# Optimization experiments

Measured on AMD Instinct MI355X. Metric: run time of the kernel, lower is better.

The kernel has to match this reference:

```python
import jax, jax.numpy as jnp
import numpy as np

N = 1024
OBS_RADIUS = 0.5


def setup_inputs() -> dict:
    key = jax.random.key(0)
    ks = jax.random.split(key, 16)
    def w(k, shape, fan_in):
        return jax.random.normal(k, shape, dtype=jnp.float32) / np.sqrt(fan_in).astype(np.float32)
    return {
        "s": jax.random.normal(ks[0], (N, 4), dtype=jnp.float32),
        "g": jax.random.normal(ks[1], (N, 2), dtype=jnp.float32),
        "conv1_w": w(ks[2], (64, 5), 5),   "conv1_b": jnp.zeros((64,), jnp.float32),
        "conv2_w": w(ks[3], (128, 64), 64), "conv2_b": jnp.zeros((128,), jnp.float32),
        "fc1_w": w(ks[4], (64, 132), 132), "fc1_b": jnp.zeros((64,), jnp.float32),
        "fc2_w": w(ks[5], (128, 64), 64),  "fc2_b": jnp.zeros((128,), jnp.float32),
        "fc3_w": w(ks[6], (64, 128), 128), "fc3_b": jnp.zeros((64,), jnp.float32),
        "fc4_w": w(ks[7], (4, 64), 64),    "fc4_b": jnp.zeros((4,), jnp.float32),
    }


def reference(s, g, conv1_w, conv1_b, conv2_w, conv2_b,
              fc1_w, fc1_b, fc2_w, fc2_b, fc3_w, fc3_b, fc4_w, fc4_b):
    n = s.shape[0]
    # pairwise agent diff + identity channel: [n, n, 5]
    pd = s[:, None, :] - s[None, :, :]
    x = jnp.concatenate([pd, jnp.eye(n, dtype=s.dtype)[:, :, None]], axis=2)
    # neighbor mask from positional distance: [n, n, 1]
    dist = jnp.linalg.norm(x[:, :, :2], axis=2, keepdims=True)
    mask = (dist < OBS_RADIUS).astype(s.dtype)
    # 1x1-conv edge MLPs (pointwise over the j dim): [n, n, 64] -> [n, n, 128]
    h = jax.nn.relu(jnp.einsum('ijc,oc->ijo', x, conv1_w) + conv1_b)
    h = jax.nn.relu(jnp.einsum('ijc,oc->ijo', h, conv2_w) + conv2_b)
    # masked max-pool over neighbors j: [n, 128]
    pooled = jnp.max(h * mask, axis=1)
    sg = s[:, :2] - g
    feat = jnp.concatenate([pooled, sg, s[:, 2:]], axis=1)  # [n, 132]
    z = jax.nn.relu(feat @ fc1_w.T + fc1_b)
    z = jax.nn.relu(z @ fc2_w.T + fc2_b)
    z = jax.nn.relu(z @ fc3_w.T + fc3_b)
    k = 2.0 * jax.nn.sigmoid(z @ fc4_w.T + fc4_b) - 1.0  # [n, 4]
    k1, k2, k3, k4 = k[:, 0:1], k[:, 1:2], k[:, 2:3], k[:, 3:4]
    zr = jnp.zeros_like(k1)
    gain_x = -jnp.concatenate([k1, zr, k2, zr], axis=1)
    gain_y = -jnp.concatenate([zr, k3, zr, k4], axis=1)
    state = jnp.concatenate([sg, s[:, 2:]], axis=1)  # [n, 4]
    a_x = jnp.sum(state * gain_x, axis=1, keepdims=True)
    a_y = jnp.sum(state * gain_y, axis=1, keepdims=True)
    return jnp.concatenate([a_x, a_y], axis=1)  # [n, 2]
```

## Files before the change

### kernel.cpp

```cpp
#include <hip/hip_runtime.h>

typedef unsigned int u32;
typedef unsigned short u16;
typedef _Float16 f16;
typedef f16 f16x8 __attribute__((ext_vector_type(8)));
typedef float f32x4 __attribute__((ext_vector_type(4)));

#define SH1 72

__global__ __launch_bounds__(64) void NetworkAction_86131274154571_kernel(
    const float* __restrict__ s,    const float* __restrict__ g,
    const float* __restrict__ w1g,  const float* __restrict__ b1g,
    const float* __restrict__ w2g,  const float* __restrict__ b2g,
    const float* __restrict__ fc1w, const float* __restrict__ fc1b,
    const float* __restrict__ fc2w, const float* __restrict__ fc2b,
    const float* __restrict__ fc3w, const float* __restrict__ fc3b,
    const float* __restrict__ fc4w, const float* __restrict__ fc4b,
    float2* __restrict__ out)
{
    __shared__ float4 actx[1024];
    __shared__ float  actf[1024];
    __shared__ f16    h1buf[16][SH1];
    __shared__ float  feat[132];
    __shared__ float  z1[64];
    __shared__ float  z2[128];
    __shared__ float  z3[64];
    __shared__ float  kk[4];

    const int lane = threadIdx.x;
    const int i    = blockIdx.x;
    const int ncol = lane & 15;
    const int kq   = lane >> 4;

    const float4 si = ((const float4*)s)[i];

    const float* wp1 = w1g + lane * 5;
    const float w10 = wp1[0], w11 = wp1[1], w12 = wp1[2], w13 = wp1[3], w14 = wp1[4];
    const float b1r = b1g[lane];

    f16x8 bfrag[8][2];
    float b2r[8];
    #pragma unroll
    for (int tile = 0; tile < 8; ++tile) {
        const int n = tile * 16 + ncol;
        b2r[tile] = b2g[n];
        #pragma unroll
        for (int t = 0; t < 2; ++t) {
            const float* wp = w2g + n * 64 + t * 32 + kq * 8;
            float4 lo = ((const float4*)wp)[0];
            float4 hi = ((const float4*)wp)[1];
            f16x8 b;
            b[0] = (f16)lo.x; b[1] = (f16)lo.y; b[2] = (f16)lo.z; b[3] = (f16)lo.w;
            b[4] = (f16)hi.x; b[5] = (f16)hi.y; b[6] = (f16)hi.z; b[7] = (f16)hi.w;
            bfrag[tile][t] = b;
        }
    }

    int cnt = 0;
    #pragma unroll
    for (int it = 0; it < 16; ++it) {
        const int j = it * 64 + lane;
        float4 sj = ((const float4*)s)[j];
        float dx = si.x - sj.x, dy = si.y - sj.y;
        bool act = (dx * dx + dy * dy) < 0.25f;
        unsigned long long m = __ballot(act);
        if (act) {
            int pos = cnt + (int)__popcll(m & ((1ull << lane) - 1ull));
            actx[pos] = make_float4(dx, dy, si.z - sj.z, si.w - sj.w);
            actf[pos] = (j == i) ? 1.0f : 0.0f;
        }
        cnt += (int)__popcll(m);
    }
    const int n_act = cnt;
    __syncthreads();

    float mt[8];
    #pragma unroll
    for (int t = 0; t < 8; ++t) mt[t] = 0.0f;

    for (int gbase = 0; gbase < n_act; gbase += 16) {
        #pragma unroll
        for (int p = 0; p < 16; ++p) {
            if (gbase + p < n_act) {
                const float4 x  = actx[gbase + p];
                const float  x4 = actf[gbase + p];
                float h = b1r;
                h = fmaf(w10, x.x, h); h = fmaf(w11, x.y, h);
                h = fmaf(w12, x.z, h); h = fmaf(w13, x.w, h);
                h = fmaf(w14, x4,  h);
                h1buf[p][lane] = (f16)fmaxf(h, 0.0f);
            }
        }
        __syncthreads();

        f16x8 afr[2];
        #pragma unroll
        for (int t = 0; t < 2; ++t)
            afr[t] = *(const f16x8*)&h1buf[ncol][t * 32 + kq * 8];

        #pragma unroll
        for (int tile = 0; tile < 8; ++tile) {
            f32x4 acc = {0.0f, 0.0f, 0.0f, 0.0f};
            acc = __builtin_amdgcn_mfma_f32_16x16x32_f16(afr[0], bfrag[tile][0], acc, 0, 0, 0);
            acc = __builtin_amdgcn_mfma_f32_16x16x32_f16(afr[1], bfrag[tile][1], acc, 0, 0, 0);
            #pragma unroll
            for (int r = 0; r < 4; ++r) {
                const bool valid = (gbase + kq * 4 + r) < n_act;
                const float v = acc[r] + b2r[tile];
                mt[tile] = valid ? fmaxf(mt[tile], v) : mt[tile];
            }
        }
        __syncthreads();
    }

    #pragma unroll
    for (int tile = 0; tile < 8; ++tile) {
        float m = mt[tile];
        m = fmaxf(m, __shfl_xor(m, 16));
        m = fmaxf(m, __shfl_xor(m, 32));
        if (lane < 16) feat[tile * 16 + lane] = m;
    }
    if (lane == 0) {
        float2 gi = ((const float2*)g)[i];
        feat[128] = si.x - gi.x;
        feat[129] = si.y - gi.y;
        feat[130] = si.z;
        feat[131] = si.w;
    }
    __syncthreads();

    {
        float a0 = fc1b[lane], a1 = 0.f, a2 = 0.f, a3 = 0.f;
        const float4* wv = (const float4*)(fc1w + lane * 132);
        #pragma unroll
        for (int q = 0; q < 33; ++q) {
            float4 u = wv[q];
            const int k = q * 4;
            float* a = (q & 3) == 0 ? &a0 : (q & 3) == 1 ? &a1 : (q & 3) == 2 ? &a2 : &a3;
            *a = fmaf(u.x, feat[k + 0], *a);
            *a = fmaf(u.y, feat[k + 1], *a);
            *a = fmaf(u.z, feat[k + 2], *a);
            *a = fmaf(u.w, feat[k + 3], *a);
        }
        z1[lane] = fmaxf((a0 + a1) + (a2 + a3), 0.0f);
    }
    __syncthreads();

    {
        float aA0 = fc2b[lane],      aA1 = 0.f;
        float aB0 = fc2b[lane + 64], aB1 = 0.f;
        const float4* wvA = (const float4*)(fc2w + lane * 64);
        const float4* wvB = (const float4*)(fc2w + (lane + 64) * 64);
        #pragma unroll
        for (int q = 0; q < 16; ++q) {
            float4 uA = wvA[q];
            float4 uB = wvB[q];
            const int k = q * 4;
            const float f0 = z1[k + 0], f1 = z1[k + 1], f2 = z1[k + 2], f3 = z1[k + 3];
            if (q & 1) {
                aA1 = fmaf(uA.x, f0, aA1); aA1 = fmaf(uA.y, f1, aA1);
                aA1 = fmaf(uA.z, f2, aA1); aA1 = fmaf(uA.w, f3, aA1);
                aB1 = fmaf(uB.x, f0, aB1); aB1 = fmaf(uB.y, f1, aB1);
                aB1 = fmaf(uB.z, f2, aB1); aB1 = fmaf(uB.w, f3, aB1);
            } else {
                aA0 = fmaf(uA.x, f0, aA0); aA0 = fmaf(uA.y, f1, aA0);
                aA0 = fmaf(uA.z, f2, aA0); aA0 = fmaf(uA.w, f3, aA0);
                aB0 = fmaf(uB.x, f0, aB0); aB0 = fmaf(uB.y, f1, aB0);
                aB0 = fmaf(uB.z, f2, aB0); aB0 = fmaf(uB.w, f3, aB0);
            }
        }
        z2[lane]      = fmaxf(aA0 + aA1, 0.0f);
        z2[lane + 64] = fmaxf(aB0 + aB1, 0.0f);
    }
    __syncthreads();

    {
        float a0 = fc3b[lane], a1 = 0.f, a2 = 0.f, a3 = 0.f;
        const float4* wv = (const float4*)(fc3w + lane * 128);
        #pragma unroll
        for (int q = 0; q < 32; ++q) {
            float4 u = wv[q];
            const int k = q * 4;
            float* a = (q & 3) == 0 ? &a0 : (q & 3) == 1 ? &a1 : (q & 3) == 2 ? &a2 : &a3;
            *a = fmaf(u.x, z2[k + 0], *a);
            *a = fmaf(u.y, z2[k + 1], *a);
            *a = fmaf(u.z, z2[k + 2], *a);
            *a = fmaf(u.w, z2[k + 3], *a);
        }
        z3[lane] = fmaxf((a0 + a1) + (a2 + a3), 0.0f);
    }
    __syncthreads();

    {
        const int q  = lane >> 4;
        const int ks = lane & 15;
        float4 u = ((const float4*)(fc4w + q * 64))[ks];
        float part = u.x * z3[ks * 4 + 0] + u.y * z3[ks * 4 + 1]
                   + u.z * z3[ks * 4 + 2] + u.w * z3[ks * 4 + 3];
        part += __shfl_xor(part, 1);
        part += __shfl_xor(part, 2);
        part += __shfl_xor(part, 4);
        part += __shfl_xor(part, 8);
        if (ks == 0)
            kk[q] = 2.0f / (1.0f + expf(-(part + fc4b[q]))) - 1.0f;
    }
    __syncthreads();

    if (lane == 0) {
        float ax = -(kk[0] * feat[128] + kk[1] * feat[130]);
        float ay = -(kk[2] * feat[129] + kk[3] * feat[131]);
        out[i] = make_float2(ax, ay);
    }
}

extern "C" void kernel_launch(void* const* d_in, const int* in_sizes, int n_in,
                              void* d_out, int out_size, void* d_ws, size_t ws_size,
                              hipStream_t stream) {
    const float* s    = (const float*)d_in[0];
    const float* g    = (const float*)d_in[1];
    const float* c1w  = (const float*)d_in[2];
    const float* c1b  = (const float*)d_in[3];
    const float* c2w  = (const float*)d_in[4];
    const float* c2b  = (const float*)d_in[5];
    const float* fc1w = (const float*)d_in[6];
    const float* fc1b = (const float*)d_in[7];
    const float* fc2w = (const float*)d_in[8];
    const float* fc2b = (const float*)d_in[9];
    const float* fc3w = (const float*)d_in[10];
    const float* fc3b = (const float*)d_in[11];
    const float* fc4w = (const float*)d_in[12];
    const float* fc4b = (const float*)d_in[13];

    float2* out = (float2*)d_out;

    NetworkAction_86131274154571_kernel<<<1024, 64, 0, stream>>>(
        s, g, c1w, c1b, c2w, c2b, fc1w, fc1b, fc2w, fc2b,
        fc3w, fc3b, fc4w, fc4b, out);
}
```

Before: 105.6 us.

## Split neighbor scan across four waves with shared fp16 conv2 weights

Each block now launches four waves. Each wave scans a quarter of the candidate neighbors, compacts them into its own slice, and runs its own MFMA edge-MLP loop. Conv2 weights are converted to fp16 once into shared memory and read from there instead of being held as per-lane register fragments. Partial max-pools are combined through shared memory, after which wave 0 alone runs the FC head, using lgkmcnt waits and shuffles in place of block barriers. Work per row is spread over more waves, at the cost of extra LDS traffic for the B fragments and an idle three waves during the FC tail.

New measurement: 104.4 us. Within noise of the previous version (-1.2%).

```diff
diff --git a/kernel.cpp b/kernel.cpp
--- a/kernel.cpp
+++ b/kernel.cpp
@@ -6,9 +6,11 @@
 typedef f16 f16x8 __attribute__((ext_vector_type(8)));
 typedef float f32x4 __attribute__((ext_vector_type(4)));
 
+#define NTH 256
 #define SH1 72
-
-__global__ __launch_bounds__(64) void NetworkAction_86131274154571_kernel(
+#define SW2 72
+
+__global__ __launch_bounds__(NTH) void NetworkAction_86131274154571_kernel(
     const float* __restrict__ s,    const float* __restrict__ g,
     const float* __restrict__ w1g,  const float* __restrict__ b1g,
     const float* __restrict__ w2g,  const float* __restrict__ b2g,
@@ -19,71 +21,78 @@
     float2* __restrict__ out)
 {
     __shared__ float4 actx[1024];
-    __shared__ float  actf[1024];
-    __shared__ f16    h1buf[16][SH1];
+    __shared__ f16    w2s[128][SW2];
+    __shared__ f16    h1all[4][16][SH1];
+    __shared__ float  pmax[4][128];
+    __shared__ int    diagslot[4];
     __shared__ float  feat[132];
     __shared__ float  z1[64];
     __shared__ float  z2[128];
     __shared__ float  z3[64];
-    __shared__ float  kk[4];
-
-    const int lane = threadIdx.x;
+
+    const int tid  = threadIdx.x;
+    const int lane = tid & 63;
+    const int wave = tid >> 6;
     const int i    = blockIdx.x;
     const int ncol = lane & 15;
     const int kq   = lane >> 4;
 
     const float4 si = ((const float4*)s)[i];
 
+    if (lane == 0) diagslot[wave] = -1;
+
+    {
+        const int n = tid >> 1, h = tid & 1;
+        const float4* wp = (const float4*)(w2g + n * 64 + h * 32);
+        #pragma unroll
+        for (int q = 0; q < 8; q += 2) {
+            float4 u0 = wp[q], u1 = wp[q + 1];
+            f16x8 b;
+            b[0] = (f16)u0.x; b[1] = (f16)u0.y; b[2] = (f16)u0.z; b[3] = (f16)u0.w;
+            b[4] = (f16)u1.x; b[5] = (f16)u1.y; b[6] = (f16)u1.z; b[7] = (f16)u1.w;
+            *(f16x8*)&w2s[n][h * 32 + q * 4] = b;
+        }
+    }
+
     const float* wp1 = w1g + lane * 5;
     const float w10 = wp1[0], w11 = wp1[1], w12 = wp1[2], w13 = wp1[3], w14 = wp1[4];
     const float b1r = b1g[lane];
-
-    f16x8 bfrag[8][2];
     float b2r[8];
     #pragma unroll
-    for (int tile = 0; tile < 8; ++tile) {
-        const int n = tile * 16 + ncol;
-        b2r[tile] = b2g[n];
-        #pragma unroll
-        for (int t = 0; t < 2; ++t) {
-            const float* wp = w2g + n * 64 + t * 32 + kq * 8;
-            float4 lo = ((const float4*)wp)[0];
-            float4 hi = ((const float4*)wp)[1];
-            f16x8 b;
-            b[0] = (f16)lo.x; b[1] = (f16)lo.y; b[2] = (f16)lo.z; b[3] = (f16)lo.w;
-            b[4] = (f16)hi.x; b[5] = (f16)hi.y; b[6] = (f16)hi.z; b[7] = (f16)hi.w;
-            bfrag[tile][t] = b;
-        }
-    }
+    for (int t = 0; t < 8; ++t) b2r[t] = b2g[t * 16 + ncol];
 
     int cnt = 0;
-    #pragma unroll
-    for (int it = 0; it < 16; ++it) {
-        const int j = it * 64 + lane;
+    const int jbase = wave * 256;
+    #pragma unroll
+    for (int it = 0; it < 4; ++it) {
+        const int j = jbase + it * 64 + lane;
         float4 sj = ((const float4*)s)[j];
         float dx = si.x - sj.x, dy = si.y - sj.y;
         bool act = (dx * dx + dy * dy) < 0.25f;
         unsigned long long m = __ballot(act);
         if (act) {
             int pos = cnt + (int)__popcll(m & ((1ull << lane) - 1ull));
-            actx[pos] = make_float4(dx, dy, si.z - sj.z, si.w - sj.w);
-            actf[pos] = (j == i) ? 1.0f : 0.0f;
+            actx[jbase + pos] = make_float4(dx, dy, si.z - sj.z, si.w - sj.w);
+            if (j == i) diagslot[wave] = pos;
         }
         cnt += (int)__popcll(m);
     }
-    const int n_act = cnt;
     __syncthreads();
 
+    const int dslot = diagslot[wave];
+    const float4* actw = &actx[jbase];
+    f16 (*h1buf)[SH1] = h1all[wave];
+
     float mt[8];
     #pragma unroll
     for (int t = 0; t < 8; ++t) mt[t] = 0.0f;
 
-    for (int gbase = 0; gbase < n_act; gbase += 16) {
+    for (int gbase = 0; gbase < cnt; gbase += 16) {
         #pragma unroll
         for (int p = 0; p < 16; ++p) {
-            if (gbase + p < n_act) {
-                const float4 x  = actx[gbase + p];
-                const float  x4 = actf[gbase + p];
+            if (gbase + p < cnt) {
+                const float4 x  = actw[gbase + p];
+                const float  x4 = (gbase + p == dslot) ? 1.0f : 0.0f;
                 float h = b1r;
                 h = fmaf(w10, x.x, h); h = fmaf(w11, x.y, h);
                 h = fmaf(w12, x.z, h); h = fmaf(w13, x.w, h);
@@ -91,26 +100,26 @@
                 h1buf[p][lane] = (f16)fmaxf(h, 0.0f);
             }
         }
-        __syncthreads();
-
-        f16x8 afr[2];
-        #pragma unroll
-        for (int t = 0; t < 2; ++t)
-            afr[t] = *(const f16x8*)&h1buf[ncol][t * 32 + kq * 8];
+        asm volatile("s_waitcnt lgkmcnt(0)" ::: "memory");
+
+        f16x8 afr0 = *(const f16x8*)&h1buf[ncol][kq * 8];
+        f16x8 afr1 = *(const f16x8*)&h1buf[ncol][32 + kq * 8];
 
         #pragma unroll
         for (int tile = 0; tile < 8; ++tile) {
+            const int n = tile * 16 + ncol;
+            f16x8 b0 = *(const f16x8*)&w2s[n][kq * 8];
+            f16x8 b1 = *(const f16x8*)&w2s[n][32 + kq * 8];
             f32x4 acc = {0.0f, 0.0f, 0.0f, 0.0f};
-            acc = __builtin_amdgcn_mfma_f32_16x16x32_f16(afr[0], bfrag[tile][0], acc, 0, 0, 0);
-            acc = __builtin_amdgcn_mfma_f32_16x16x32_f16(afr[1], bfrag[tile][1], acc, 0, 0, 0);
+            acc = __builtin_amdgcn_mfma_f32_16x16x32_f16(afr0, b0, acc, 0, 0, 0);
+            acc = __builtin_amdgcn_mfma_f32_16x16x32_f16(afr1, b1, acc, 0, 0, 0);
             #pragma unroll
             for (int r = 0; r < 4; ++r) {
-                const bool valid = (gbase + kq * 4 + r) < n_act;
+                const bool valid = (gbase + kq * 4 + r) < cnt;
                 const float v = acc[r] + b2r[tile];
                 mt[tile] = valid ? fmaxf(mt[tile], v) : mt[tile];
             }
         }
-        __syncthreads();
     }
 
     #pragma unroll
@@ -118,16 +127,25 @@
         float m = mt[tile];
         m = fmaxf(m, __shfl_xor(m, 16));
         m = fmaxf(m, __shfl_xor(m, 32));
-        if (lane < 16) feat[tile * 16 + lane] = m;
-    }
+        if (lane < 16) pmax[wave][tile * 16 + lane] = m;
+    }
+    __syncthreads();
+    if (wave != 0) return;
+
+    {
+        float m0 = fmaxf(fmaxf(pmax[0][lane],      pmax[1][lane]),
+                         fmaxf(pmax[2][lane],      pmax[3][lane]));
+        float m1 = fmaxf(fmaxf(pmax[0][lane + 64], pmax[1][lane + 64]),
+                         fmaxf(pmax[2][lane + 64], pmax[3][lane + 64]));
+        feat[lane]      = m0;
+        feat[lane + 64] = m1;
+    }
+    const float2 gi = ((const float2*)g)[i];
+    const float sgx = si.x - gi.x, sgy = si.y - gi.y;
     if (lane == 0) {
-        float2 gi = ((const float2*)g)[i];
-        feat[128] = si.x - gi.x;
-        feat[129] = si.y - gi.y;
-        feat[130] = si.z;
-        feat[131] = si.w;
-    }
-    __syncthreads();
+        feat[128] = sgx; feat[129] = sgy; feat[130] = si.z; feat[131] = si.w;
+    }
+    asm volatile("s_waitcnt lgkmcnt(0)" ::: "memory");
 
     {
         float a0 = fc1b[lane], a1 = 0.f, a2 = 0.f, a3 = 0.f;
@@ -144,7 +162,7 @@
         }
         z1[lane] = fmaxf((a0 + a1) + (a2 + a3), 0.0f);
     }
-    __syncthreads();
+    asm volatile("s_waitcnt lgkmcnt(0)" ::: "memory");
 
     {
         float aA0 = fc2b[lane],      aA1 = 0.f;
@@ -172,7 +190,7 @@
         z2[lane]      = fmaxf(aA0 + aA1, 0.0f);
         z2[lane + 64] = fmaxf(aB0 + aB1, 0.0f);
     }
-    __syncthreads();
+    asm volatile("s_waitcnt lgkmcnt(0)" ::: "memory");
 
     {
         float a0 = fc3b[lane], a1 = 0.f, a2 = 0.f, a3 = 0.f;
@@ -189,7 +207,7 @@
         }
         z3[lane] = fmaxf((a0 + a1) + (a2 + a3), 0.0f);
     }
-    __syncthreads();
+    asm volatile("s_waitcnt lgkmcnt(0)" ::: "memory");
 
     {
         const int q  = lane >> 4;
@@ -201,15 +219,16 @@
         part += __shfl_xor(part, 2);
         part += __shfl_xor(part, 4);
         part += __shfl_xor(part, 8);
-        if (ks == 0)
-            kk[q] = 2.0f / (1.0f + expf(-(part + fc4b[q]))) - 1.0f;
-    }
-    __syncthreads();
-
-    if (lane == 0) {
-        float ax = -(kk[0] * feat[128] + kk[1] * feat[130]);
-        float ay = -(kk[2] * feat[129] + kk[3] * feat[131]);
-        out[i] = make_float2(ax, ay);
+        const float kv = 2.0f / (1.0f + expf(-(part + fc4b[q]))) - 1.0f;
+        const float k0 = __shfl(kv, 0);
+        const float k1 = __shfl(kv, 16);
+        const float k2 = __shfl(kv, 32);
+        const float k3 = __shfl(kv, 48);
+        if (lane == 0) {
+            float ax = -(k0 * sgx + k1 * si.z);
+            float ay = -(k2 * sgy + k3 * si.w);
+            out[i] = make_float2(ax, ay);
+        }
     }
 }
 
@@ -233,7 +252,7 @@
 
     float2* out = (float2*)d_out;
 
-    NetworkAction_86131274154571_kernel<<<1024, 64, 0, stream>>>(
+    NetworkAction_86131274154571_kernel<<<1024, NTH, 0, stream>>>(
         s, g, c1w, c1b, c2w, c2b, fc1w, fc1b, fc2w, fc2b,
         fc3w, fc3b, fc4w, fc4b, out);
 }
```

## Split edge MLP across four waves per block with double-buffered h1 staging

Applied to the files above, without the earlier changes.

Raises the block from one wave to four, so each wave owns 32 of the 128 conv2 output channels. The layer-1 computation for each group of 16 neighbors is spread over all 256 threads, each computing two channels from shared-memory weights. The h1 buffer is double-buffered so one barrier per group can be dropped. Neighbor compaction now uses a shared atomic counter instead of a wave ballot, and the diagonal slot is tracked rather than stored per entry. After pooling, the tail MLP runs on wave 0 only, using s_waitcnt instead of barriers and shuffles for the final gains. Per-block work is cut and occupancy raised, at the cost of more block-wide syncs and atomic contention.

After: 99.86 us. -5.5%, faster.

```diff
diff --git a/kernel.cpp b/kernel.cpp
--- a/kernel.cpp
+++ b/kernel.cpp
@@ -6,9 +6,10 @@
 typedef f16 f16x8 __attribute__((ext_vector_type(8)));
 typedef float f32x4 __attribute__((ext_vector_type(4)));
 
+#define NTH 256
 #define SH1 72
 
-__global__ __launch_bounds__(64) void NetworkAction_86131274154571_kernel(
+__global__ __launch_bounds__(NTH) void NetworkAction_86131274154571_kernel(
     const float* __restrict__ s,    const float* __restrict__ g,
     const float* __restrict__ w1g,  const float* __restrict__ b1g,
     const float* __restrict__ w2g,  const float* __restrict__ b2g,
@@ -19,30 +20,35 @@
     float2* __restrict__ out)
 {
     __shared__ float4 actx[1024];
-    __shared__ float  actf[1024];
-    __shared__ f16    h1buf[16][SH1];
+    __shared__ f16    h1buf[2][16][SH1];
+    __shared__ float  w1s[320];
+    __shared__ float  b1s[64];
     __shared__ float  feat[132];
     __shared__ float  z1[64];
     __shared__ float  z2[128];
     __shared__ float  z3[64];
-    __shared__ float  kk[4];
-
-    const int lane = threadIdx.x;
+    __shared__ int    cnt;
+    __shared__ int    diagslot;
+
+    const int tid  = threadIdx.x;
+    const int lane = tid & 63;
+    const int wave = tid >> 6;
     const int i    = blockIdx.x;
     const int ncol = lane & 15;
     const int kq   = lane >> 4;
 
+    if (tid == 0) cnt = 0;
+    for (int q = tid; q < 320; q += NTH) w1s[q] = w1g[q];
+    if (tid < 64) b1s[tid] = b1g[tid];
+
     const float4 si = ((const float4*)s)[i];
 
-    const float* wp1 = w1g + lane * 5;
-    const float w10 = wp1[0], w11 = wp1[1], w12 = wp1[2], w13 = wp1[3], w14 = wp1[4];
-    const float b1r = b1g[lane];
-
-    f16x8 bfrag[8][2];
-    float b2r[8];
+    const int n_base = wave * 32;
+    f16x8 bfrag[2][2];
+    float b2r[2];
     #pragma unroll
-    for (int tile = 0; tile < 8; ++tile) {
-        const int n = tile * 16 + ncol;
+    for (int tile = 0; tile < 2; ++tile) {
+        const int n = n_base + tile * 16 + ncol;
         b2r[tile] = b2g[n];
         #pragma unroll
         for (int t = 0; t < 2; ++t) {
@@ -55,79 +61,85 @@
             bfrag[tile][t] = b;
         }
     }
-
-    int cnt = 0;
+    __syncthreads();
+
     #pragma unroll
-    for (int it = 0; it < 16; ++it) {
-        const int j = it * 64 + lane;
+    for (int p = 0; p < 4; ++p) {
+        const int j = p * NTH + tid;
         float4 sj = ((const float4*)s)[j];
         float dx = si.x - sj.x, dy = si.y - sj.y;
-        bool act = (dx * dx + dy * dy) < 0.25f;
-        unsigned long long m = __ballot(act);
-        if (act) {
-            int pos = cnt + (int)__popcll(m & ((1ull << lane) - 1ull));
-            actx[pos] = make_float4(dx, dy, si.z - sj.z, si.w - sj.w);
-            actf[pos] = (j == i) ? 1.0f : 0.0f;
-        }
-        cnt += (int)__popcll(m);
-    }
+        if (dx * dx + dy * dy < 0.25f) {
+            int slot = atomicAdd(&cnt, 1);
+            actx[slot] = make_float4(dx, dy, si.z - sj.z, si.w - sj.w);
+            if (j == i) diagslot = slot;
+        }
+    }
+    __syncthreads();
     const int n_act = cnt;
-    __syncthreads();
-
-    float mt[8];
-    #pragma unroll
-    for (int t = 0; t < 8; ++t) mt[t] = 0.0f;
+    const int dslot = diagslot;
+
+    float mtile[2] = {0.0f, 0.0f};
 
     for (int gbase = 0; gbase < n_act; gbase += 16) {
-        #pragma unroll
-        for (int p = 0; p < 16; ++p) {
+        const int bufI = (gbase >> 4) & 1;
+        #pragma unroll
+        for (int it = 0; it < 2; ++it) {
+            const int idx = it * NTH + tid;
+            const int p = idx >> 5, c2 = idx & 31;
             if (gbase + p < n_act) {
                 const float4 x  = actx[gbase + p];
-                const float  x4 = actf[gbase + p];
-                float h = b1r;
-                h = fmaf(w10, x.x, h); h = fmaf(w11, x.y, h);
-                h = fmaf(w12, x.z, h); h = fmaf(w13, x.w, h);
-                h = fmaf(w14, x4,  h);
-                h1buf[p][lane] = (f16)fmaxf(h, 0.0f);
+                const float  x4 = (gbase + p == dslot) ? 1.0f : 0.0f;
+                const int c = c2 * 2;
+                const float* wa = &w1s[c * 5];
+                float ha = b1s[c];
+                ha = fmaf(wa[0], x.x, ha); ha = fmaf(wa[1], x.y, ha);
+                ha = fmaf(wa[2], x.z, ha); ha = fmaf(wa[3], x.w, ha);
+                ha = fmaf(wa[4], x4,  ha);
+                const float* wb = &w1s[c * 5 + 5];
+                float hb = b1s[c + 1];
+                hb = fmaf(wb[0], x.x, hb); hb = fmaf(wb[1], x.y, hb);
+                hb = fmaf(wb[2], x.z, hb); hb = fmaf(wb[3], x.w, hb);
+                hb = fmaf(wb[4], x4,  hb);
+                f16 fa = (f16)fmaxf(ha, 0.0f);
+                f16 fb = (f16)fmaxf(hb, 0.0f);
+                u32 pk = (u32)__builtin_bit_cast(u16, fa) |
+                         ((u32)__builtin_bit_cast(u16, fb) << 16);
+                *(u32*)&h1buf[bufI][p][c2 * 2] = pk;
             }
         }
         __syncthreads();
 
-        f16x8 afr[2];
-        #pragma unroll
-        for (int t = 0; t < 2; ++t)
-            afr[t] = *(const f16x8*)&h1buf[ncol][t * 32 + kq * 8];
-
-        #pragma unroll
-        for (int tile = 0; tile < 8; ++tile) {
+        f16x8 afr0 = *(const f16x8*)&h1buf[bufI][ncol][kq * 8];
+        f16x8 afr1 = *(const f16x8*)&h1buf[bufI][ncol][32 + kq * 8];
+
+        #pragma unroll
+        for (int tile = 0; tile < 2; ++tile) {
             f32x4 acc = {0.0f, 0.0f, 0.0f, 0.0f};
-            acc = __builtin_amdgcn_mfma_f32_16x16x32_f16(afr[0], bfrag[tile][0], acc, 0, 0, 0);
-            acc = __builtin_amdgcn_mfma_f32_16x16x32_f16(afr[1], bfrag[tile][1], acc, 0, 0, 0);
+            acc = __builtin_amdgcn_mfma_f32_16x16x32_f16(afr0, bfrag[tile][0], acc, 0, 0, 0);
+            acc = __builtin_amdgcn_mfma_f32_16x16x32_f16(afr1, bfrag[tile][1], acc, 0, 0, 0);
             #pragma unroll
             for (int r = 0; r < 4; ++r) {
                 const bool valid = (gbase + kq * 4 + r) < n_act;
                 const float v = acc[r] + b2r[tile];
-                mt[tile] = valid ? fmaxf(mt[tile], v) : mt[tile];
+                mtile[tile] = valid ? fmaxf(mtile[tile], v) : mtile[tile];
             }
         }
-        __syncthreads();
     }
 
     #pragma unroll
-    for (int tile = 0; tile < 8; ++tile) {
-        float m = mt[tile];
+    for (int tile = 0; tile < 2; ++tile) {
+        float m = mtile[tile];
         m = fmaxf(m, __shfl_xor(m, 16));
         m = fmaxf(m, __shfl_xor(m, 32));
-        if (lane < 16) feat[tile * 16 + lane] = m;
-    }
-    if (lane == 0) {
-        float2 gi = ((const float2*)g)[i];
-        feat[128] = si.x - gi.x;
-        feat[129] = si.y - gi.y;
-        feat[130] = si.z;
-        feat[131] = si.w;
+        if (lane < 16) feat[n_base + tile * 16 + lane] = m;
+    }
+    const float2 gi = ((const float2*)g)[i];
+    const float sgx = si.x - gi.x, sgy = si.y - gi.y;
+    if (tid == 0) {
+        feat[128] = sgx; feat[129] = sgy; feat[130] = si.z; feat[131] = si.w;
     }
     __syncthreads();
+    if (wave != 0) return;
 
     {
         float a0 = fc1b[lane], a1 = 0.f, a2 = 0.f, a3 = 0.f;
@@ -144,7 +156,7 @@
         }
         z1[lane] = fmaxf((a0 + a1) + (a2 + a3), 0.0f);
     }
-    __syncthreads();
+    asm volatile("s_waitcnt lgkmcnt(0)" ::: "memory");
 
     {
         float aA0 = fc2b[lane],      aA1 = 0.f;
@@ -172,7 +184,7 @@
         z2[lane]      = fmaxf(aA0 + aA1, 0.0f);
         z2[lane + 64] = fmaxf(aB0 + aB1, 0.0f);
     }
-    __syncthreads();
+    asm volatile("s_waitcnt lgkmcnt(0)" ::: "memory");
 
     {
         float a0 = fc3b[lane], a1 = 0.f, a2 = 0.f, a3 = 0.f;
@@ -189,7 +201,7 @@
         }
         z3[lane] = fmaxf((a0 + a1) + (a2 + a3), 0.0f);
     }
-    __syncthreads();
+    asm volatile("s_waitcnt lgkmcnt(0)" ::: "memory");
 
     {
         const int q  = lane >> 4;
@@ -201,15 +213,16 @@
         part += __shfl_xor(part, 2);
         part += __shfl_xor(part, 4);
         part += __shfl_xor(part, 8);
-        if (ks == 0)
-            kk[q] = 2.0f / (1.0f + expf(-(part + fc4b[q]))) - 1.0f;
-    }
-    __syncthreads();
-
-    if (lane == 0) {
-        float ax = -(kk[0] * feat[128] + kk[1] * feat[130]);
-        float ay = -(kk[2] * feat[129] + kk[3] * feat[131]);
-        out[i] = make_float2(ax, ay);
+        const float kv = 2.0f / (1.0f + expf(-(part + fc4b[q]))) - 1.0f;
+        const float k0 = __shfl(kv, 0);
+        const float k1 = __shfl(kv, 16);
+        const float k2 = __shfl(kv, 32);
+        const float k3 = __shfl(kv, 48);
+        if (lane == 0) {
+            float ax = -(k0 * sgx + k1 * si.z);
+            float ay = -(k2 * sgy + k3 * si.w);
+            out[i] = make_float2(ax, ay);
+        }
     }
 }
 
@@ -233,7 +246,7 @@
 
     float2* out = (float2*)d_out;
 
-    NetworkAction_86131274154571_kernel<<<1024, 64, 0, stream>>>(
+    NetworkAction_86131274154571_kernel<<<1024, NTH, 0, stream>>>(
         s, g, c1w, c1b, c2w, c2b, fc1w, fc1b, fc2w, fc2b,
         fc3w, fc3b, fc4w, fc4b, out);
 }
```
